# Optimization experiments

Hardware: AMD Instinct MI355X
Metric: run time of the kernel (lower is better)

The kernel has to match this reference:

```python
import math
import jax, jax.numpy as jnp
import numpy as np

B_, L_, D_, N_, R_ = 4, 1024, 1024, 16, 64  # batch, seq, n_embd(=dim_inner), d_state, dt_rank


def setup_inputs() -> dict:
    key = jax.random.key(0)
    ks = jax.random.split(key, 6)
    s = lambda k, shp: jax.random.normal(k, shp, jnp.float32) * 0.02
    return {
        "x": jax.random.normal(ks[0], (B_, L_, D_), jnp.float32),
        "ln1_w": jnp.ones((D_,), jnp.float32),
        "ln2_w": jnp.ones((D_,), jnp.float32),
        "W_dbc": s(ks[1], (R_ + 2 * N_, D_)),   # x -> [delta_lowrank, B, C]
        "W_dt": s(ks[2], (D_, R_)),              # dt_rank -> dim_inner
        "b_dt": jnp.zeros((D_,), jnp.float32),
        "A_log": jnp.log(jnp.broadcast_to(jnp.arange(1, N_ + 1, dtype=jnp.float32), (D_, N_))),
        "Dp": jnp.ones((D_,), jnp.float32),      # skip-connection D parameter
        "W_fc": s(ks[3], (4 * D_, D_)),
        "W_proj": s(ks[4], (D_, 4 * D_)),
    }


def _layernorm(x, w):
    mu = jnp.mean(x, -1, keepdims=True)
    xc = x - mu
    var = jnp.mean(xc * xc, -1, keepdims=True)
    return xc * jax.lax.rsqrt(var + 1e-5) * w


def _new_gelu(x):
    c = math.sqrt(2.0 / math.pi)
    return 0.5 * x * (1.0 + jnp.tanh(c * (x + 0.044715 * x * x * x)))


def _ssm(x, W_dbc, W_dt, b_dt, A_log, Dp):
    # x: (b, l, d) with d == dim_inner == n_embd
    dbc = jnp.einsum("bld,ed->ble", x, W_dbc)                # (b,l,R+2N)
    delta, Bm, Cm = jnp.split(dbc, [R_, R_ + N_], axis=-1)
    delta = jax.nn.softplus(jnp.einsum("blr,dr->bld", delta, W_dt) + b_dt)  # (b,l,d)
    A = -jnp.exp(A_log)                                       # (d,n)
    dA = jnp.exp(delta[..., None] * A)                        # (b,l,d,n) discretized A
    dBx = (delta * x)[..., None] * Bm[:, :, None, :]          # (b,l,d,n) discretized B*x

    # h_t = dA_t * h_{t-1} + dBx_t  -> parallel first-order linear scan
    def combine(e1, e2):
        a1, b1 = e1
        a2, b2 = e2
        return a2 * a1, a2 * b1 + b2

    _, hs = jax.lax.associative_scan(combine, (dA, dBx), axis=1)
    y = jnp.einsum("bldn,bln->bld", hs, Cm)
    return y + x * Dp


def reference(x, ln1_w, ln2_w, W_dbc, W_dt, b_dt, A_log, Dp, W_fc, W_proj):
    h = jax.nn.softplus(_layernorm(x, ln1_w))
    h = h + _ssm(h, W_dbc, W_dt, b_dt, A_log, Dp)
    m = _layernorm(h, ln2_w)
    m = _new_gelu(jnp.einsum("bld,fd->blf", m, W_fc))
    m = jnp.einsum("blf,df->bld", m, W_proj)
    return h + m
```

## Files before the change

kernel.cpp:

```cpp
#include <hip/hip_runtime.h>
#include <cstdint>
#include <cstddef>

typedef unsigned short u16;
typedef unsigned int u32;
typedef __attribute__((ext_vector_type(8))) short short8;
typedef __attribute__((ext_vector_type(4))) float floatx4;
typedef __attribute__((ext_vector_type(4))) u16 u16x4;

#define DEV static __device__ __forceinline__

DEV u16 f2b(float f){ u32 u = __float_as_uint(f); u32 r = u + 0x7fffu + ((u>>16)&1u); return (u16)(r>>16); }
DEV float softplusf(float z){ return fmaxf(z,0.f) + log1pf(__expf(-fabsf(z))); }
DEV float fast_tanhf(float u){ float e = __expf(2.f*u); return 1.f - 2.f/(e+1.f); }
DEV float geluf(float x){ float u = 0.7978845608028654f*(x + 0.044715f*x*x*x); return 0.5f*x*(1.f+fast_tanhf(u)); }

DEV void async_copy16(const void* gp, void* lp){
  __builtin_amdgcn_global_load_lds((const __attribute__((address_space(1))) u32*)gp,
                                   (__attribute__((address_space(3))) u32*)lp, 16, 0, 0);
}

__global__ void cast_kernel(const float* __restrict__ src, u16* __restrict__ dst, int n){
  int i = blockIdx.x*256 + threadIdx.x;
  if (i < n) dst[i] = f2b(src[i]);
}

__global__ void cast4_kernel(const float* __restrict__ src, u16* __restrict__ dst, int n4){
  int i = blockIdx.x*256 + threadIdx.x;
  if (i < n4){
    float4 v = ((const float4*)src)[i];
    u16x4 o = { f2b(v.x), f2b(v.y), f2b(v.z), f2b(v.w) };
    *(u16x4*)(dst + i*4) = o;
  }
}

__global__ void cast_dbc_pad(const float* __restrict__ src, u16* __restrict__ dst){
  int i = blockIdx.x*256 + threadIdx.x;
  int r = i >> 10;
  dst[i] = (r < 96) ? f2b(src[i]) : (u16)0;
}

__global__ void dbc_post(const float* __restrict__ p, u16* __restrict__ delta_in,
                         float* __restrict__ BCf){
  int e = blockIdx.x*256 + threadIdx.x;
  int t = e >> 7, c = e & 127;
  float s = 0.f;
  #pragma unroll
  for (int z=0;z<8;z++) s += p[(size_t)z*524288 + e];
  if (c < 64)      delta_in[t*64 + c] = f2b(s);
  else if (c < 96) BCf[t*32 + (c-64)] = s;
}

__global__ void proj_reduce(const float* __restrict__ p, const float* __restrict__ h1f,
                            float* __restrict__ out){
  int i = blockIdx.x*256 + threadIdx.x;
  float4 a = ((const float4*)p)[i];
  float4 b = ((const float4*)(p + (size_t)4194304))[i];
  float4 r = ((const float4*)h1f)[i];
  float4 o = make_float4(a.x+b.x+r.x, a.y+b.y+r.y, a.z+b.z+r.z, a.w+b.w+r.w);
  ((float4*)out)[i] = o;
}

__global__ __launch_bounds__(256)
void ln1_kernel(const float* __restrict__ x, const float* __restrict__ w,
                float* __restrict__ h0f, u16* __restrict__ h0b)
{
  int row = blockIdx.x, tid = threadIdx.x;
  const float4* xr = (const float4*)(x + (size_t)row*1024);
  float4 v = xr[tid];
  float s1 = v.x+v.y+v.z+v.w;
  float s2 = v.x*v.x+v.y*v.y+v.z*v.z+v.w*v.w;
  #pragma unroll
  for (int m=1;m<64;m<<=1){ s1 += __shfl_xor(s1,m); s2 += __shfl_xor(s2,m); }
  __shared__ float red[8];
  int wv = tid>>6;
  if ((tid&63)==0){ red[wv]=s1; red[4+wv]=s2; }
  __syncthreads();
  s1 = red[0]+red[1]+red[2]+red[3];
  s2 = red[4]+red[5]+red[6]+red[7];
  float mu  = s1*(1.f/1024.f);
  float var = s2*(1.f/1024.f) - mu*mu;
  float rstd = rsqrtf(var + 1e-5f);
  float4 wv4 = ((const float4*)w)[tid];
  float o0 = softplusf((v.x-mu)*rstd*wv4.x);
  float o1 = softplusf((v.y-mu)*rstd*wv4.y);
  float o2 = softplusf((v.z-mu)*rstd*wv4.z);
  float o3 = softplusf((v.w-mu)*rstd*wv4.w);
  ((float4*)(h0f + (size_t)row*1024))[tid] = make_float4(o0,o1,o2,o3);
  u16x4 ob = { f2b(o0), f2b(o1), f2b(o2), f2b(o3) };
  *(u16x4*)(h0b + (size_t)row*1024 + tid*4) = ob;
}

__global__ __launch_bounds__(256)
void ln2_kernel(const float* __restrict__ x, const float* __restrict__ w,
                u16* __restrict__ outb)
{
  int row = blockIdx.x, tid = threadIdx.x;
  const float4* xr = (const float4*)(x + (size_t)row*1024);
  float4 v = xr[tid];
  float s1 = v.x+v.y+v.z+v.w;
  float s2 = v.x*v.x+v.y*v.y+v.z*v.z+v.w*v.w;
  #pragma unroll
  for (int m=1;m<64;m<<=1){ s1 += __shfl_xor(s1,m); s2 += __shfl_xor(s2,m); }
  __shared__ float red[8];
  int wv = tid>>6;
  if ((tid&63)==0){ red[wv]=s1; red[4+wv]=s2; }
  __syncthreads();
  s1 = red[0]+red[1]+red[2]+red[3];
  s2 = red[4]+red[5]+red[6]+red[7];
  float mu  = s1*(1.f/1024.f);
  float var = s2*(1.f/1024.f) - mu*mu;
  float rstd = rsqrtf(var + 1e-5f);
  float4 wv4 = ((const float4*)w)[tid];
  u16x4 ob = { f2b((v.x-mu)*rstd*wv4.x), f2b((v.y-mu)*rstd*wv4.y),
               f2b((v.z-mu)*rstd*wv4.z), f2b((v.w-mu)*rstd*wv4.w) };
  *(u16x4*)(outb + (size_t)row*1024 + tid*4) = ob;
}

template<int EPI>
__global__ __launch_bounds__(256)
void gemm_bt(const u16* __restrict__ A, int lda,
             const u16* __restrict__ B, int ldb, int K,
             float* __restrict__ outF, u16* __restrict__ outB, int ldo,
             const float* __restrict__ bias, size_t zstr)
{
  __shared__ u16 sA[128*32];
  __shared__ u16 sB[128*32];
  const int tid = threadIdx.x;
  const int m0 = blockIdx.y * 128, n0 = blockIdx.x * 128;
  const int kstart = blockIdx.z * K;
  const int wave = tid>>6, lane = tid&63;
  const int wm = (wave>>1)*64, wn = (wave&1)*64;
  const int lr = lane&15, quad = lane>>4;

  floatx4 acc[4][4];
  #pragma unroll
  for (int i=0;i<4;i++)
    #pragma unroll
    for (int j=0;j<4;j++){ floatx4 z = {0.f,0.f,0.f,0.f}; acc[i][j]=z; }

  const int r0 = tid>>2;
  const int kc8 = (((tid&3) ^ ((tid>>3)&3)))*8;
  const int sswz = ((lr>>1)&3);
  for (int k0=kstart; k0<kstart+K; k0+=32){
    __syncthreads();
    async_copy16(A + (size_t)(m0+r0)*lda    + k0+kc8, &sA[(size_t)tid*8]);
    async_copy16(A + (size_t)(m0+64+r0)*lda + k0+kc8, &sA[(size_t)(tid+256)*8]);
    async_copy16(B + (size_t)(n0+r0)*ldb    + k0+kc8, &sB[(size_t)tid*8]);
    async_copy16(B + (size_t)(n0+64+r0)*ldb + k0+kc8, &sB[(size_t)(tid+256)*8]);
    __syncthreads();
    short8 af[4], bf[4];
    #pragma unroll
    for (int i=0;i<4;i++){
      af[i] = *(const short8*)&sA[(wm+i*16+lr)*32 + (quad^sswz)*8];
      bf[i] = *(const short8*)&sB[(wn+i*16+lr)*32 + (quad^sswz)*8];
    }
    #pragma unroll
    for (int i=0;i<4;i++)
      #pragma unroll
      for (int j=0;j<4;j++)
        acc[i][j] = __builtin_amdgcn_mfma_f32_16x16x32_bf16(af[i], bf[j], acc[i][j], 0,0,0);
  }
  #pragma unroll
  for (int i=0;i<4;i++){
    #pragma unroll
    for (int j=0;j<4;j++){
      #pragma unroll
      for (int r=0;r<4;r++){
        int gr = m0 + wm + i*16 + quad*4 + r;
        int gc = n0 + wn + j*16 + lr;
        float v = acc[i][j][r];
        size_t o = (size_t)gr*ldo + gc;
        if (EPI==1)      outF[o] = softplusf(v + bias[gc]);
        else if (EPI==2) outB[o] = f2b(geluf(v));
        else             outF[zstr*blockIdx.z + o] = v;
      }
    }
  }
}

__global__ __launch_bounds__(256)
void scan_p1(const float* __restrict__ delta, const float* __restrict__ h0f,
             const float* __restrict__ BCf, const float* __restrict__ A_log,
             float* __restrict__ Pbuf, float* __restrict__ Sbuf)
{
  int blk = blockIdx.x;
  int d = (blk & 3)*256 + threadIdx.x;
  int c = (blk >> 2) & 63;
  int b = blk >> 8;
  float a2[16], h[16], P[16];
  #pragma unroll
  for (int n=0;n<16;n++){ a2[n] = -__expf(A_log[d*16+n]) * 1.44269504f; h[n]=0.f; P[n]=1.f; }
  int t0 = c*16;
  const float* dptr = delta + ((size_t)(b*1024 + t0))*1024 + d;
  const float* xptr = h0f   + ((size_t)(b*1024 + t0))*1024 + d;
  const float* bc   = BCf   + ((size_t)(b*1024 + t0))*32;
  #pragma unroll 4
  for (int t=0;t<16;t++){
    float dlt = dptr[t*1024];
    float xv  = xptr[t*1024];
    float dx = dlt*xv;
    #pragma unroll
    for (int n=0;n<16;n++){
      float dA = exp2f(dlt*a2[n]);
      h[n] = dA*h[n] + dx*bc[t*32+n];
      P[n] *= dA;
    }
  }
  size_t base = ((size_t)((b*64 + c)*16))*1024 + d;
  #pragma unroll
  for (int n=0;n<16;n++){ Pbuf[base + (size_t)n*1024] = P[n]; Sbuf[base + (size_t)n*1024] = h[n]; }
}

__global__ __launch_bounds__(256)
void scan_p2(const float* __restrict__ Pbuf, const float* __restrict__ Sbuf,
             float* __restrict__ Hbuf)
{
  int blk = blockIdx.x;
  int d = (blk & 3)*256 + threadIdx.x;
  int n = (blk >> 2) & 15;
  int b = blk >> 6;
  float H = 0.f;
  for (int c=0;c<64;c++){
    size_t idx = ((size_t)((b*64 + c)*16 + n))*1024 + d;
    float P = Pbuf[idx], S = Sbuf[idx];
    Hbuf[idx] = H;
    H = P*H + S;
  }
}

__global__ __launch_bounds__(256)
void scan_p3(const float* __restrict__ delta, const float* __restrict__ h0f,
             const float* __restrict__ BCf, const float* __restrict__ A_log,
             const float* __restrict__ Hbuf, const float* __restrict__ Dp,
             float* __restrict__ h1f)
{
  int blk = blockIdx.x;
  int d = (blk & 3)*256 + threadIdx.x;
  int c = (blk >> 2) & 63;
  int b = blk >> 8;
  float a2[16], h[16];
  size_t hb = ((size_t)((b*64 + c)*16))*1024 + d;
  #pragma unroll
  for (int n=0;n<16;n++){
    a2[n] = -__expf(A_log[d*16+n]) * 1.44269504f;
    h[n] = Hbuf[hb + (size_t)n*1024];
  }
  float dpv = 1.f + Dp[d];
  int t0 = c*16;
  const float* dptr = delta + ((size_t)(b*1024 + t0))*1024 + d;
  const float* xptr = h0f   + ((size_t)(b*1024 + t0))*1024 + d;
  const float* bc   = BCf   + ((size_t)(b*1024 + t0))*32;
  float* optr = h1f + ((size_t)(b*1024 + t0))*1024 + d;
  #pragma unroll 4
  for (int t=0;t<16;t++){
    float dlt = dptr[t*1024];
    float xv  = xptr[t*1024];
    float dx = dlt*xv;
    float y = 0.f;
    #pragma unroll
    for (int n=0;n<16;n++){
      float dA = exp2f(dlt*a2[n]);
      h[n] = dA*h[n] + dx*bc[t*32+n];
      y += h[n]*bc[t*32+16+n];
    }
    optr[t*1024] = xv*dpv + y;
  }
}

extern "C" void kernel_launch(void* const* d_in, const int* in_sizes, int n_in,
                              void* d_out, int out_size, void* d_ws, size_t ws_size,
                              hipStream_t stream)
{
  const float* x    = (const float*)d_in[0];
  const float* ln1w = (const float*)d_in[1];
  const float* ln2w = (const float*)d_in[2];
  const float* Wdbc = (const float*)d_in[3];
  const float* Wdt  = (const float*)d_in[4];
  const float* bdt  = (const float*)d_in[5];
  const float* Alog = (const float*)d_in[6];
  const float* Dp   = (const float*)d_in[7];
  const float* Wfc  = (const float*)d_in[8];
  const float* Wproj= (const float*)d_in[9];
  float* out = (float*)d_out;

  char* ws = (char*)d_ws;
  size_t off = 0;
  auto carve = [&](size_t bytes)->char*{ char* p = ws + off; off += (bytes + 255) & ~(size_t)255; return p; };
  const size_t T = 4096;
  float* h0f   = (float*)carve(T*1024*4);
  float* h1f   = (float*)carve(T*1024*4);
  float* dlt   = (float*)carve(T*1024*4);
  float* Pbuf  = (float*)carve((size_t)4*64*16*1024*4);
  float* Sbuf  = (float*)carve((size_t)4*64*16*1024*4);
  float* Hbuf  = (float*)carve((size_t)4*64*16*1024*4);
  float* BCf   = (float*)carve(T*32*4);
  u16*   h0b   = (u16*)  carve(T*1024*2);
  u16*   m0b   = (u16*)  carve(T*1024*2);
  u16*   g_b   = (u16*)  carve(T*4096*2);
  u16*   din_b = (u16*)  carve(T*64*2);
  u16*   Wdbc_b= (u16*)  carve((size_t)128*1024*2);
  u16*   Wdt_b = (u16*)  carve((size_t)1024*64*2);
  u16*   Wfc_b = (u16*)  carve((size_t)4096*1024*2);
  u16*   Wpj_b = (u16*)  carve((size_t)1024*4096*2);
  float* dbc_p  = Hbuf;
  float* proj_p = Pbuf;
  (void)ws_size; (void)in_sizes; (void)n_in; (void)out_size;

  cast_dbc_pad<<<512, 256, 0, stream>>>(Wdbc, Wdbc_b);
  cast_kernel <<<256, 256, 0, stream>>>(Wdt, Wdt_b, 1024*64);
  cast4_kernel<<<4096,256, 0, stream>>>(Wfc, Wfc_b, 4096*1024/4);
  cast4_kernel<<<4096,256, 0, stream>>>(Wproj, Wpj_b, 1024*4096/4);

  ln1_kernel<<<4096, 256, 0, stream>>>(x, ln1w, h0f, h0b);

  gemm_bt<4><<<dim3(1,32,8), 256, 0, stream>>>(h0b, 1024, Wdbc_b, 1024, 128,
                                               dbc_p, nullptr, 128, nullptr, (size_t)T*128);
  dbc_post<<<2048, 256, 0, stream>>>(dbc_p, din_b, BCf);

  gemm_bt<1><<<dim3(8,32), 256, 0, stream>>>(din_b, 64, Wdt_b, 64, 64,
                                             dlt, nullptr, 1024, bdt, 0);

  scan_p1<<<1024, 256, 0, stream>>>(dlt, h0f, BCf, Alog, Pbuf, Sbuf);
  scan_p2<<<256,  256, 0, stream>>>(Pbuf, Sbuf, Hbuf);
  scan_p3<<<1024, 256, 0, stream>>>(dlt, h0f, BCf, Alog, Hbuf, Dp, h1f);

  ln2_kernel<<<4096, 256, 0, stream>>>(h1f, ln2w, m0b);

  gemm_bt<2><<<dim3(32,32), 256, 0, stream>>>(m0b, 1024, Wfc_b, 1024, 1024,
                                              nullptr, g_b, 4096, nullptr, 0);

  gemm_bt<4><<<dim3(8,32,2), 256, 0, stream>>>(g_b, 4096, Wpj_b, 4096, 2048,
                                               proj_p, nullptr, 1024, nullptr, (size_t)T*1024);
  proj_reduce<<<4096, 256, 0, stream>>>(proj_p, h1f, out);
}
```

Baseline: 364.7 us.

## Fuse weight casts, add XCD-aware GEMM block swizzle, lengthen scan chunks

```diff
diff --git a/kernel.cpp b/kernel.cpp
--- a/kernel.cpp
+++ b/kernel.cpp
@@ -20,24 +20,24 @@
                                    (__attribute__((address_space(3))) u32*)lp, 16, 0, 0);
 }
 
-__global__ void cast_kernel(const float* __restrict__ src, u16* __restrict__ dst, int n){
+__global__ __launch_bounds__(256)
+void prep_weights(const float* __restrict__ Wdbc, const float* __restrict__ Wdt,
+                  const float* __restrict__ Wfc, const float* __restrict__ Wproj,
+                  u16* __restrict__ dbc_b, u16* __restrict__ dt_b,
+                  u16* __restrict__ fc_b, u16* __restrict__ pj_b)
+{
   int i = blockIdx.x*256 + threadIdx.x;
-  if (i < n) dst[i] = f2b(src[i]);
-}
-
-__global__ void cast4_kernel(const float* __restrict__ src, u16* __restrict__ dst, int n4){
-  int i = blockIdx.x*256 + threadIdx.x;
-  if (i < n4){
-    float4 v = ((const float4*)src)[i];
-    u16x4 o = { f2b(v.x), f2b(v.y), f2b(v.z), f2b(v.w) };
-    *(u16x4*)(dst + i*4) = o;
-  }
-}
-
-__global__ void cast_dbc_pad(const float* __restrict__ src, u16* __restrict__ dst){
-  int i = blockIdx.x*256 + threadIdx.x;
-  int r = i >> 10;
-  dst[i] = (r < 96) ? f2b(src[i]) : (u16)0;
+  const float* src; u16* dst; int j;
+  if (i < 32768){
+    int e = i*4, r = e >> 10;
+    if (r >= 96){ u16x4 z = {0,0,0,0}; *(u16x4*)(dbc_b + e) = z; return; }
+    src = Wdbc; dst = dbc_b; j = i;
+  } else if (i < 49152){ src = Wdt;   dst = dt_b; j = i - 32768; }
+  else if (i < 1097728){ src = Wfc;   dst = fc_b; j = i - 49152; }
+  else                 { src = Wproj; dst = pj_b; j = i - 1097728; }
+  float4 v = ((const float4*)src)[j];
+  u16x4 o = { f2b(v.x), f2b(v.y), f2b(v.z), f2b(v.w) };
+  *(u16x4*)(dst + j*4) = o;
 }
 
 __global__ void dbc_post(const float* __restrict__ p, u16* __restrict__ delta_in,
@@ -117,7 +117,7 @@
   *(u16x4*)(outb + (size_t)row*1024 + tid*4) = ob;
 }
 
-template<int EPI>
+template<int EPI, int SWZ>
 __global__ __launch_bounds__(256)
 void gemm_bt(const u16* __restrict__ A, int lda,
              const u16* __restrict__ B, int ldb, int K,
@@ -127,8 +127,21 @@
   __shared__ u16 sA[128*32];
   __shared__ u16 sB[128*32];
   const int tid = threadIdx.x;
-  const int m0 = blockIdx.y * 128, n0 = blockIdx.x * 128;
-  const int kstart = blockIdx.z * K;
+  int m_blk, n_blk, zb;
+  if (SWZ == 0){ n_blk = blockIdx.x; m_blk = blockIdx.y; zb = blockIdx.z; }
+  else if (SWZ == 1){
+    int b = blockIdx.x, xcd = b & 7, local = b >> 3;
+    m_blk = (xcd>>2)*16 + (local & 15);
+    n_blk = (xcd&3)*8 + (local >> 4);
+    zb = 0;
+  } else {
+    int b = blockIdx.x, xcd = b & 7, local = b >> 3;
+    m_blk = (xcd>>1)*8 + (local & 7);
+    n_blk = local >> 3;
+    zb = xcd & 1;
+  }
+  const int m0 = m_blk*128, n0 = n_blk*128;
+  const int kstart = zb * K;
   const int wave = tid>>6, lane = tid&63;
   const int wm = (wave>>1)*64, wn = (wave&1)*64;
   const int lr = lane&15, quad = lane>>4;
@@ -173,7 +186,7 @@
         size_t o = (size_t)gr*ldo + gc;
         if (EPI==1)      outF[o] = softplusf(v + bias[gc]);
         else if (EPI==2) outB[o] = f2b(geluf(v));
-        else             outF[zstr*blockIdx.z + o] = v;
+        else             outF[zstr*zb + o] = v;
       }
     }
   }
@@ -186,17 +199,17 @@
 {
   int blk = blockIdx.x;
   int d = (blk & 3)*256 + threadIdx.x;
-  int c = (blk >> 2) & 63;
-  int b = blk >> 8;
+  int c = (blk >> 2) & 31;
+  int b = blk >> 7;
   float a2[16], h[16], P[16];
   #pragma unroll
   for (int n=0;n<16;n++){ a2[n] = -__expf(A_log[d*16+n]) * 1.44269504f; h[n]=0.f; P[n]=1.f; }
-  int t0 = c*16;
+  int t0 = c*32;
   const float* dptr = delta + ((size_t)(b*1024 + t0))*1024 + d;
   const float* xptr = h0f   + ((size_t)(b*1024 + t0))*1024 + d;
   const float* bc   = BCf   + ((size_t)(b*1024 + t0))*32;
   #pragma unroll 4
-  for (int t=0;t<16;t++){
+  for (int t=0;t<32;t++){
     float dlt = dptr[t*1024];
     float xv  = xptr[t*1024];
     float dx = dlt*xv;
@@ -207,7 +220,7 @@
       P[n] *= dA;
     }
   }
-  size_t base = ((size_t)((b*64 + c)*16))*1024 + d;
+  size_t base = ((size_t)((b*32 + c)*16))*1024 + d;
   #pragma unroll
   for (int n=0;n<16;n++){ Pbuf[base + (size_t)n*1024] = P[n]; Sbuf[base + (size_t)n*1024] = h[n]; }
 }
@@ -221,8 +234,8 @@
   int n = (blk >> 2) & 15;
   int b = blk >> 6;
   float H = 0.f;
-  for (int c=0;c<64;c++){
-    size_t idx = ((size_t)((b*64 + c)*16 + n))*1024 + d;
+  for (int c=0;c<32;c++){
+    size_t idx = ((size_t)((b*32 + c)*16 + n))*1024 + d;
     float P = Pbuf[idx], S = Sbuf[idx];
     Hbuf[idx] = H;
     H = P*H + S;
@@ -237,23 +250,23 @@
 {
   int blk = blockIdx.x;
   int d = (blk & 3)*256 + threadIdx.x;
-  int c = (blk >> 2) & 63;
-  int b = blk >> 8;
+  int c = (blk >> 2) & 31;
+  int b = blk >> 7;
   float a2[16], h[16];
-  size_t hb = ((size_t)((b*64 + c)*16))*1024 + d;
+  size_t hb = ((size_t)((b*32 + c)*16))*1024 + d;
   #pragma unroll
   for (int n=0;n<16;n++){
     a2[n] = -__expf(A_log[d*16+n]) * 1.44269504f;
     h[n] = Hbuf[hb + (size_t)n*1024];
   }
   float dpv = 1.f + Dp[d];
-  int t0 = c*16;
+  int t0 = c*32;
   const float* dptr = delta + ((size_t)(b*1024 + t0))*1024 + d;
   const float* xptr = h0f   + ((size_t)(b*1024 + t0))*1024 + d;
   const float* bc   = BCf   + ((size_t)(b*1024 + t0))*32;
   float* optr = h1f + ((size_t)(b*1024 + t0))*1024 + d;
   #pragma unroll 4
-  for (int t=0;t<16;t++){
+  for (int t=0;t<32;t++){
     float dlt = dptr[t*1024];
     float xv  = xptr[t*1024];
     float dx = dlt*xv;
@@ -291,9 +304,10 @@
   float* h0f   = (float*)carve(T*1024*4);
   float* h1f   = (float*)carve(T*1024*4);
   float* dlt   = (float*)carve(T*1024*4);
-  float* Pbuf  = (float*)carve((size_t)4*64*16*1024*4);
-  float* Sbuf  = (float*)carve((size_t)4*64*16*1024*4);
-  float* Hbuf  = (float*)carve((size_t)4*64*16*1024*4);
+  float* Pbuf  = (float*)carve((size_t)4*32*16*1024*4);
+  float* Sbuf  = (float*)carve((size_t)4*32*16*1024*4);
+  float* Hbuf  = (float*)carve((size_t)4*32*16*1024*4);
+  float* pad_  = (float*)carve((size_t)4*32*16*1024*4);
   float* BCf   = (float*)carve(T*32*4);
   u16*   h0b   = (u16*)  carve(T*1024*2);
   u16*   m0b   = (u16*)  carve(T*1024*2);
@@ -305,32 +319,30 @@
   u16*   Wpj_b = (u16*)  carve((size_t)1024*4096*2);
   float* dbc_p  = Hbuf;
   float* proj_p = Pbuf;
-  (void)ws_size; (void)in_sizes; (void)n_in; (void)out_size;
-
-  cast_dbc_pad<<<512, 256, 0, stream>>>(Wdbc, Wdbc_b);
-  cast_kernel <<<256, 256, 0, stream>>>(Wdt, Wdt_b, 1024*64);
-  cast4_kernel<<<4096,256, 0, stream>>>(Wfc, Wfc_b, 4096*1024/4);
-  cast4_kernel<<<4096,256, 0, stream>>>(Wproj, Wpj_b, 1024*4096/4);
+  (void)pad_; (void)ws_size; (void)in_sizes; (void)n_in; (void)out_size;
+
+  prep_weights<<<8384, 256, 0, stream>>>(Wdbc, Wdt, Wfc, Wproj,
+                                         Wdbc_b, Wdt_b, Wfc_b, Wpj_b);
 
   ln1_kernel<<<4096, 256, 0, stream>>>(x, ln1w, h0f, h0b);
 
-  gemm_bt<4><<<dim3(1,32,8), 256, 0, stream>>>(h0b, 1024, Wdbc_b, 1024, 128,
-                                               dbc_p, nullptr, 128, nullptr, (size_t)T*128);
+  gemm_bt<4,0><<<dim3(1,32,8), 256, 0, stream>>>(h0b, 1024, Wdbc_b, 1024, 128,
+                                                 dbc_p, nullptr, 128, nullptr, (size_t)T*128);
   dbc_post<<<2048, 256, 0, stream>>>(dbc_p, din_b, BCf);
 
-  gemm_bt<1><<<dim3(8,32), 256, 0, stream>>>(din_b, 64, Wdt_b, 64, 64,
-                                             dlt, nullptr, 1024, bdt, 0);
-
-  scan_p1<<<1024, 256, 0, stream>>>(dlt, h0f, BCf, Alog, Pbuf, Sbuf);
-  scan_p2<<<256,  256, 0, stream>>>(Pbuf, Sbuf, Hbuf);
-  scan_p3<<<1024, 256, 0, stream>>>(dlt, h0f, BCf, Alog, Hbuf, Dp, h1f);
+  gemm_bt<1,0><<<dim3(8,32), 256, 0, stream>>>(din_b, 64, Wdt_b, 64, 64,
+                                               dlt, nullptr, 1024, bdt, 0);
+
+  scan_p1<<<512, 256, 0, stream>>>(dlt, h0f, BCf, Alog, Pbuf, Sbuf);
+  scan_p2<<<256, 256, 0, stream>>>(Pbuf, Sbuf, Hbuf);
+  scan_p3<<<512, 256, 0, stream>>>(dlt, h0f, BCf, Alog, Hbuf, Dp, h1f);
 
   ln2_kernel<<<4096, 256, 0, stream>>>(h1f, ln2w, m0b);
 
-  gemm_bt<2><<<dim3(32,32), 256, 0, stream>>>(m0b, 1024, Wfc_b, 1024, 1024,
-                                              nullptr, g_b, 4096, nullptr, 0);
-
-  gemm_bt<4><<<dim3(8,32,2), 256, 0, stream>>>(g_b, 4096, Wpj_b, 4096, 2048,
-                                               proj_p, nullptr, 1024, nullptr, (size_t)T*1024);
+  gemm_bt<2,1><<<1024, 256, 0, stream>>>(m0b, 1024, Wfc_b, 1024, 1024,
+                                         nullptr, g_b, 4096, nullptr, 0);
+
+  gemm_bt<4,2><<<512, 256, 0, stream>>>(g_b, 4096, Wpj_b, 4096, 2048,
+                                        proj_p, nullptr, 1024, nullptr, (size_t)T*1024);
   proj_reduce<<<4096, 256, 0, stream>>>(proj_p, h1f, out);
 }
```

After: 356.7 us. 2.2% less time.
